# Optimization experiments

Measured on AMD Instinct MI355X. Metric: run time of the kernel, lower is better.

The kernel has to match this reference:

```python
import jax, jax.numpy as jnp
import numpy as np

B, T, XS, HS = 256, 512, 256, 256


def setup_inputs() -> dict:
    key = jax.random.key(0)
    ks = jax.random.split(key, 9)
    scale_x = np.sqrt(6.0 / (XS + HS)).astype(np.float32)  # xavier_uniform-like scale
    scale_h = np.sqrt(6.0 / (HS + HS)).astype(np.float32)
    d = {"x": jax.random.normal(ks[0], (B, T, XS), dtype=jnp.float32)}
    names = ["i", "f", "g", "o"]
    for n, kx, kh in zip(names, ks[1:5], ks[5:9]):
        d[f"wx_{n}"] = jax.random.uniform(kx, (XS, HS), jnp.float32, -scale_x, scale_x)
        d[f"wh_{n}"] = jax.random.uniform(kh, (HS, HS), jnp.float32, -scale_h, scale_h)
        d[f"bx_{n}"] = jnp.zeros((HS,), jnp.float32)
        d[f"bh_{n}"] = jnp.zeros((HS,), jnp.float32)
    return d


def reference(x, wx_i, bx_i, wh_i, bh_i, wx_f, bx_f, wh_f, bh_f,
              wx_g, bx_g, wh_g, bh_g, wx_o, bx_o, wh_o, bh_o):
    bs, ts, xs = x.shape
    hs = wx_i.shape[1]
    # Fuse the 4 input projections and 4 hidden projections into 2 GEMMs
    # (identical math to 8 separate matmuls).
    Wx = jnp.concatenate([wx_i, wx_f, wx_g, wx_o], axis=1)      # [xs, 4hs]
    Wh = jnp.concatenate([wh_i, wh_f, wh_g, wh_o], axis=1)      # [hs, 4hs]
    b = jnp.concatenate([bx_i + bh_i, bx_f + bh_f, bx_g + bh_g, bx_o + bh_o])

    # Precompute all input projections in one big GEMM: [bs, ts, 4hs]
    x_proj = jnp.einsum('btx,xg->btg', x, Wx) + b

    def step(carry, xt_proj):
        h, c = carry
        gates = xt_proj + h @ Wh                      # [bs, 4hs]
        i_t = jax.nn.sigmoid(gates[:, 0 * hs:1 * hs])
        f_t = jax.nn.sigmoid(gates[:, 1 * hs:2 * hs])
        g_t = jnp.tanh(gates[:, 2 * hs:3 * hs])
        o_t = jax.nn.sigmoid(gates[:, 3 * hs:4 * hs])
        c_new = f_t * c + i_t * g_t
        h_new = o_t * jnp.tanh(c_new)
        return (h_new, c_new), None

    h0 = jnp.zeros((bs, hs), x.dtype)
    c0 = jnp.zeros((bs, hs), x.dtype)
    (h_t, c_t), _ = jax.lax.scan(step, (h0, c0), jnp.swapaxes(x_proj, 0, 1))
    return (h_t, c_t)
```

## Files before the change

kernel.cpp:

```cpp
#include <hip/hip_runtime.h>
#include <hip/hip_bf16.h>

#define BB   256
#define TT   512
#define XSZ  256
#define HSZ  256

typedef __bf16 bf16_t;
typedef __attribute__((ext_vector_type(8))) __bf16 bf16x8;
typedef __attribute__((ext_vector_type(4))) float  f32x4;
typedef __attribute__((ext_vector_type(4))) unsigned uint4v;

__device__ __forceinline__ f32x4 splat4(float v) { f32x4 r = {v, v, v, v}; return r; }

__global__ void prep_bias(const float* bx0, const float* bh0, const float* bx1, const float* bh1,
                          const float* bx2, const float* bh2, const float* bx3, const float* bh3,
                          float* bias) {
  const float* bxs[4] = {bx0, bx1, bx2, bx3};
  const float* bhs[4] = {bh0, bh1, bh2, bh3};
  int g = blockIdx.x, c = threadIdx.x;
  bias[g * 256 + c] = bxs[g][c] + bhs[g][c];
}

__global__ void prep_wtf(const float* wx0, const float* wh0, const float* wx1, const float* wh1,
                         const float* wx2, const float* wh2, const float* wx3, const float* wh3,
                         bf16_t* Wtf) {
  const float* whs[4] = {wh0, wh1, wh2, wh3};
  const float* wxs[4] = {wx0, wx1, wx2, wx3};
  int id = blockIdx.x * 256 + threadIdx.x;
  int L  = id & 63;
  int kt = (id >> 6) & 15;
  int nt = (id >> 10) & 1;
  int w  = (id >> 11) & 7;
  int j  = (id >> 14) & 3;
  int tc   = L & 15;
  int gate = tc & 3;
  int hc   = j * 64 + w * 8 + nt * 4 + (tc >> 2);
  int k0   = kt * 32 + (L >> 4) * 8;
  const float* src = (k0 < 256) ? (whs[gate] + (size_t)k0 * 256 + hc)
                                : (wxs[gate] + (size_t)(k0 - 256) * 256 + hc);
  bf16x8 v;
#pragma unroll
  for (int i = 0; i < 8; ++i) v[i] = (__bf16)src[(size_t)i * 256];
  reinterpret_cast<bf16x8*>(Wtf)[id] = v;
}

__global__ void prep_xbf(const float* __restrict__ x, bf16_t* __restrict__ xb) {
  size_t id = (size_t)blockIdx.x * 256 + threadIdx.x;
  const float* p = x + id * 8;
  f32x4 lo = *reinterpret_cast<const f32x4*>(p);
  f32x4 hi = *reinterpret_cast<const f32x4*>(p + 4);
  bf16x8 v;
#pragma unroll
  for (int i = 0; i < 4; ++i) { v[i] = (__bf16)lo[i]; v[i + 4] = (__bf16)hi[i]; }
  reinterpret_cast<bf16x8*>(xb)[id] = v;
}

template <bool XBF>
__global__ __launch_bounds__(512, 2)
void lstm_seq(const void* __restrict__ xsrc, const bf16_t* __restrict__ Wtf,
              const float* __restrict__ bias, unsigned* __restrict__ hseq,
              float* __restrict__ out)
{
  __shared__ __align__(16) char hxl[2][8192];

  const int tid  = threadIdx.x;
  const int w    = tid >> 6;
  const int lane = tid & 63;
  const int l15  = lane & 15, l4 = lane >> 4;
  const int bid  = blockIdx.x;
  const int g    = bid >> 2, j = bid & 3;
  const int b0   = g * 16;
  const int gate = l15 & 3;
  const int hcg  = l15 >> 2;
  const bool isg = (gate == 2);

  const float*  xf32 = (const float*)xsrc;
  const bf16_t* xbf  = (const bf16_t*)xsrc;

  const char* wbase = (const char*)Wtf + (size_t)(j * 256 + w * 32) * 1024 + lane * 16;
  bf16x8 Bh[2][8], Bx[2][8];
#pragma unroll
  for (int nt = 0; nt < 2; ++nt)
#pragma unroll
    for (int kt = 0; kt < 8; ++kt) {
      Bh[nt][kt] = *reinterpret_cast<const bf16x8*>(wbase + (nt * 16 + kt) * 1024);
      Bx[nt][kt] = *reinterpret_cast<const bf16x8*>(wbase + (nt * 16 + 8 + kt) * 1024);
    }

  float bias_v[2];
#pragma unroll
  for (int nt = 0; nt < 2; ++nt)
    bias_v[nt] = bias[gate * 256 + j * 64 + w * 8 + nt * 4 + hcg];

  f32x4 cst0 = {0.f, 0.f, 0.f, 0.f};
  f32x4 cst1 = {0.f, 0.f, 0.f, 0.f};

  f32x4 acc_x0 = splat4(bias_v[0]);
  f32x4 acc_x1 = splat4(bias_v[1]);
#pragma unroll
  for (int k8 = 0; k8 < 8; ++k8) {
    bf16x8 a;
    if constexpr (XBF) {
      a = *reinterpret_cast<const bf16x8*>(
          xbf + (size_t)(b0 + l15) * (TT * XSZ) + k8 * 32 + l4 * 8);
    } else {
      const float* xp = xf32 + (size_t)(b0 + l15) * (TT * XSZ) + k8 * 32 + l4 * 8;
      f32x4 lo = *reinterpret_cast<const f32x4*>(xp);
      f32x4 hi = *reinterpret_cast<const f32x4*>(xp + 4);
#pragma unroll
      for (int i = 0; i < 4; ++i) { a[i] = (__bf16)lo[i]; a[i + 4] = (__bf16)hi[i]; }
    }
    acc_x0 = __builtin_amdgcn_mfma_f32_16x16x32_bf16(a, Bx[0][k8], acc_x0, 0, 0, 0);
    acc_x1 = __builtin_amdgcn_mfma_f32_16x16x32_bf16(a, Bx[1][k8], acc_x1, 0, 0, 0);
  }

#pragma unroll 1
  for (int t = 0; t < TT; ++t) {
    f32x4 acc0 = acc_x0;
    f32x4 acc1 = acc_x1;

    if (t > 0) {
      const unsigned* hp = hseq + (size_t)(t & 1) * 65536
                         + (size_t)(b0 + l15) * HSZ + w * 32 + l4 * 8;
      const unsigned tg = (unsigned)t;
      uint4v A, B;
      for (;;) {
        asm volatile("global_load_dwordx4 %0, %2, off sc0 sc1\n\t"
                     "global_load_dwordx4 %1, %2, off offset:16 sc0 sc1\n\t"
                     "s_waitcnt vmcnt(0)"
                     : "=&v"(A), "=&v"(B) : "v"(hp) : "memory");
        bool ok = ((A[0] >> 16) == tg) & ((A[1] >> 16) == tg) &
                  ((A[2] >> 16) == tg) & ((A[3] >> 16) == tg) &
                  ((B[0] >> 16) == tg) & ((B[1] >> 16) == tg) &
                  ((B[2] >> 16) == tg) & ((B[3] >> 16) == tg);
        if (__all((int)ok)) break;
        __builtin_amdgcn_s_sleep(1);
      }
      __builtin_amdgcn_sched_barrier(0);
      unsigned p0 = (A[0] & 0xFFFFu) | (A[1] << 16);
      unsigned p1 = (A[2] & 0xFFFFu) | (A[3] << 16);
      unsigned p2 = (B[0] & 0xFFFFu) | (B[1] << 16);
      unsigned p3 = (B[2] & 0xFFFFu) | (B[3] << 16);
      uint4v pk = {p0, p1, p2, p3};
      *reinterpret_cast<uint4v*>(hxl[t & 1] + w * 1024 + lane * 16) = pk;
    }
    __syncthreads();

    if (t > 0) {
#pragma unroll
      for (int kt = 0; kt < 8; ++kt) {
        bf16x8 a = *reinterpret_cast<const bf16x8*>(hxl[t & 1] + kt * 1024 + lane * 16);
        acc0 = __builtin_amdgcn_mfma_f32_16x16x32_bf16(a, Bh[0][kt], acc0, 0, 0, 0);
        acc1 = __builtin_amdgcn_mfma_f32_16x16x32_bf16(a, Bh[1][kt], acc1, 0, 0, 0);
      }
    }

    float hsel[2], csel[2];
#pragma unroll
    for (int nt = 0; nt < 2; ++nt) {
      f32x4 acc = nt ? acc1 : acc0;
      f32x4 av;
#pragma unroll
      for (int r = 0; r < 4; ++r) {
        float p = isg ? 2.f * acc[r] : acc[r];
        float s = 1.f / (1.f + __expf(-p));
        av[r] = isg ? (2.f * s - 1.f) : s;
      }
      f32x4 bv, v0, v1, c0, c1;
#pragma unroll
      for (int r = 0; r < 4; ++r) bv[r] = __shfl_xor(av[r], 1);
#pragma unroll
      for (int r = 0; r < 4; ++r) {
        v0[r] = (gate & 1) ? bv[r] : av[r];
        v1[r] = (gate & 1) ? av[r] : bv[r];
      }
#pragma unroll
      for (int r = 0; r < 4; ++r) { c0[r] = __shfl_xor(v0[r], 2); c1[r] = __shfl_xor(v1[r], 2); }
      f32x4 hv;
      f32x4 cs = nt ? cst1 : cst0;
#pragma unroll
      for (int r = 0; r < 4; ++r) {
        float iv = (gate & 2) ? c0[r] : v0[r];
        float fv = (gate & 2) ? c1[r] : v1[r];
        float gv = (gate & 2) ? v0[r] : c0[r];
        float ov = (gate & 2) ? v1[r] : c1[r];
        float cn = fv * cs[r] + iv * gv;
        cs[r] = cn;
        float s2 = 1.f / (1.f + __expf(-2.f * cn));
        hv[r] = ov * (2.f * s2 - 1.f);
      }
      if (nt) cst1 = cs; else cst0 = cs;
      float hs = (gate == 0) ? hv[0] : (gate == 1) ? hv[1] : (gate == 2) ? hv[2] : hv[3];
      float cc = (gate == 0) ? cs[0] : (gate == 1) ? cs[1] : (gate == 2) ? cs[2] : cs[3];
      hsel[nt] = hs;
      csel[nt] = cc;
    }

    if (t + 1 < TT) {
#pragma unroll
      for (int nt = 0; nt < 2; ++nt) {
        __bf16 hb16 = (__bf16)hsel[nt];
        unsigned hv = ((unsigned)(t + 1) << 16)
                    | (unsigned)__builtin_bit_cast(unsigned short, hb16);
        unsigned* hp2 = hseq + (size_t)((t + 1) & 1) * 65536
                      + (size_t)(b0 + l4 * 4 + gate) * HSZ
                      + (j * 64 + w * 8 + nt * 4 + hcg);
        asm volatile("global_store_dword %0, %1, off sc0 sc1" :: "v"(hp2), "v"(hv) : "memory");
      }

      acc_x0 = splat4(bias_v[0]);
      acc_x1 = splat4(bias_v[1]);
#pragma unroll
      for (int k8 = 0; k8 < 8; ++k8) {
        bf16x8 a;
        if constexpr (XBF) {
          a = *reinterpret_cast<const bf16x8*>(
              xbf + (size_t)(b0 + l15) * (TT * XSZ) + (size_t)(t + 1) * XSZ + k8 * 32 + l4 * 8);
        } else {
          const float* xp = xf32 + (size_t)(b0 + l15) * (TT * XSZ)
                          + (size_t)(t + 1) * XSZ + k8 * 32 + l4 * 8;
          f32x4 lo = *reinterpret_cast<const f32x4*>(xp);
          f32x4 hi = *reinterpret_cast<const f32x4*>(xp + 4);
#pragma unroll
          for (int i = 0; i < 4; ++i) { a[i] = (__bf16)lo[i]; a[i + 4] = (__bf16)hi[i]; }
        }
        acc_x0 = __builtin_amdgcn_mfma_f32_16x16x32_bf16(a, Bx[0][k8], acc_x0, 0, 0, 0);
        acc_x1 = __builtin_amdgcn_mfma_f32_16x16x32_bf16(a, Bx[1][k8], acc_x1, 0, 0, 0);
      }
    } else {
#pragma unroll
      for (int nt = 0; nt < 2; ++nt) {
        float* op = out + (size_t)(b0 + l4 * 4 + gate) * HSZ
                  + (j * 64 + w * 8 + nt * 4 + hcg);
        op[0] = hsel[nt];
        op[(size_t)BB * HSZ] = csel[nt];
      }
    }
  }
}

extern "C" void kernel_launch(void* const* d_in, const int* in_sizes, int n_in,
                              void* d_out, int out_size, void* d_ws, size_t ws_size,
                              hipStream_t stream) {
  const float* x = (const float*)d_in[0];
  const float *wx[4], *wh[4], *bx[4], *bh[4];
  for (int g = 0; g < 4; ++g) {
    wx[g] = (const float*)d_in[1 + 4 * g];
    wh[g] = (const float*)d_in[2 + 4 * g];
    bx[g] = (const float*)d_in[3 + 4 * g];
    bh[g] = (const float*)d_in[4 + 4 * g];
  }

  char* ws = (char*)d_ws;
  float*    bias = (float*)ws;
  bf16_t*   Wtf  = (bf16_t*)(ws + 4096);
  unsigned* hseq = (unsigned*)(ws + 4096 + 1048576);
  bf16_t*   xbf  = (bf16_t*)(ws + 4096 + 1048576 + 524288);
  const size_t need_xbf = 4096 + 1048576 + 524288 + (size_t)BB * TT * XSZ * 2;

  prep_bias<<<dim3(4), dim3(256), 0, stream>>>(bx[0], bh[0], bx[1], bh[1],
                                               bx[2], bh[2], bx[3], bh[3], bias);
  prep_wtf<<<dim3(256), dim3(256), 0, stream>>>(wx[0], wh[0], wx[1], wh[1],
                                                wx[2], wh[2], wx[3], wh[3], Wtf);
  if (ws_size >= need_xbf) {
    prep_xbf<<<dim3((BB * TT * XSZ / 8) / 256), dim3(256), 0, stream>>>(x, xbf);
    lstm_seq<true><<<dim3(64), dim3(512), 0, stream>>>(xbf, Wtf, bias, hseq,
                                                       (float*)d_out);
  } else {
    lstm_seq<false><<<dim3(64), dim3(512), 0, stream>>>(x, Wtf, bias, hseq,
                                                        (float*)d_out);
  }
}
```

Measured before the change: 2.227 ms.

## Split hidden dimension across 8 blocks per batch group and stage Wx in LDS

The hidden-column work is split across 8 blocks per 16-row batch group instead of 4, doubling the grid to 128 blocks so each wave handles one 16-column MFMA tile instead of two. The input-projection weights move from registers into a 64 KB LDS buffer, and accumulation alternates between two accumulators to break MFMA dependency chains. This shortens the per-step critical path. In exchange it doubles the number of producers taking part in the global-memory h exchange, adds LDS reads for Wx every step, and uses much more shared memory per block.

```diff
diff --git a/kernel.cpp b/kernel.cpp
--- a/kernel.cpp
+++ b/kernel.cpp
@@ -27,16 +27,15 @@
                          bf16_t* Wtf) {
   const float* whs[4] = {wh0, wh1, wh2, wh3};
   const float* wxs[4] = {wx0, wx1, wx2, wx3};
-  int id = blockIdx.x * 256 + threadIdx.x;
-  int L  = id & 63;
-  int kt = (id >> 6) & 15;
-  int nt = (id >> 10) & 1;
-  int w  = (id >> 11) & 7;
-  int j  = (id >> 14) & 3;
+  int id  = blockIdx.x * 256 + threadIdx.x;
+  int L   = id & 63;
+  int kts = (id >> 6) & 15;
+  int w   = (id >> 10) & 7;
+  int j   = (id >> 13) & 7;
   int tc   = L & 15;
   int gate = tc & 3;
-  int hc   = j * 64 + w * 8 + nt * 4 + (tc >> 2);
-  int k0   = kt * 32 + (L >> 4) * 8;
+  int hc   = j * 32 + w * 4 + (tc >> 2);
+  int k0   = kts * 32 + (L >> 4) * 8;
   const float* src = (k0 < 256) ? (whs[gate] + (size_t)k0 * 256 + hc)
                                 : (wxs[gate] + (size_t)(k0 - 256) * 256 + hc);
   bf16x8 v;
@@ -62,6 +61,7 @@
               const float* __restrict__ bias, unsigned* __restrict__ hseq,
               float* __restrict__ out)
 {
+  __shared__ __align__(16) char bxlds[65536];
   __shared__ __align__(16) char hxl[2][8192];
 
   const int tid  = threadIdx.x;
@@ -69,7 +69,7 @@
   const int lane = tid & 63;
   const int l15  = lane & 15, l4 = lane >> 4;
   const int bid  = blockIdx.x;
-  const int g    = bid >> 2, j = bid & 3;
+  const int g    = bid >> 3, j = bid & 7;
   const int b0   = g * 16;
   const int gate = l15 & 3;
   const int hcg  = l15 >> 2;
@@ -78,26 +78,25 @@
   const float*  xf32 = (const float*)xsrc;
   const bf16_t* xbf  = (const bf16_t*)xsrc;
 
-  const char* wbase = (const char*)Wtf + (size_t)(j * 256 + w * 32) * 1024 + lane * 16;
-  bf16x8 Bh[2][8], Bx[2][8];
-#pragma unroll
-  for (int nt = 0; nt < 2; ++nt)
-#pragma unroll
-    for (int kt = 0; kt < 8; ++kt) {
-      Bh[nt][kt] = *reinterpret_cast<const bf16x8*>(wbase + (nt * 16 + kt) * 1024);
-      Bx[nt][kt] = *reinterpret_cast<const bf16x8*>(wbase + (nt * 16 + 8 + kt) * 1024);
-    }
-
-  float bias_v[2];
-#pragma unroll
-  for (int nt = 0; nt < 2; ++nt)
-    bias_v[nt] = bias[gate * 256 + j * 64 + w * 8 + nt * 4 + hcg];
-
-  f32x4 cst0 = {0.f, 0.f, 0.f, 0.f};
-  f32x4 cst1 = {0.f, 0.f, 0.f, 0.f};
-
-  f32x4 acc_x0 = splat4(bias_v[0]);
-  f32x4 acc_x1 = splat4(bias_v[1]);
+  const char* wbase = (const char*)Wtf + ((size_t)(j * 8 + w) * 16) * 1024 + lane * 16;
+  bf16x8 Bh[8];
+#pragma unroll
+  for (int kt = 0; kt < 8; ++kt)
+    Bh[kt] = *reinterpret_cast<const bf16x8*>(wbase + kt * 1024);
+#pragma unroll
+  for (int q = 0; q < 8; ++q) {
+    bf16x8 v = *reinterpret_cast<const bf16x8*>(wbase + (8 + q) * 1024);
+    *reinterpret_cast<bf16x8*>(bxlds + (w * 8 + q) * 1024 + lane * 16) = v;
+  }
+
+  const float bias_v = bias[gate * 256 + j * 32 + w * 4 + hcg];
+
+  f32x4 cst = {0.f, 0.f, 0.f, 0.f};
+
+  __syncthreads();
+
+  f32x4 axa = splat4(bias_v);
+  f32x4 axb = {0.f, 0.f, 0.f, 0.f};
 #pragma unroll
   for (int k8 = 0; k8 < 8; ++k8) {
     bf16x8 a;
@@ -111,14 +110,15 @@
 #pragma unroll
       for (int i = 0; i < 4; ++i) { a[i] = (__bf16)lo[i]; a[i + 4] = (__bf16)hi[i]; }
     }
-    acc_x0 = __builtin_amdgcn_mfma_f32_16x16x32_bf16(a, Bx[0][k8], acc_x0, 0, 0, 0);
-    acc_x1 = __builtin_amdgcn_mfma_f32_16x16x32_bf16(a, Bx[1][k8], acc_x1, 0, 0, 0);
+    bf16x8 bx = *reinterpret_cast<const bf16x8*>(bxlds + (w * 8 + k8) * 1024 + lane * 16);
+    if (k8 & 1) axb = __builtin_amdgcn_mfma_f32_16x16x32_bf16(a, bx, axb, 0, 0, 0);
+    else        axa = __builtin_amdgcn_mfma_f32_16x16x32_bf16(a, bx, axa, 0, 0, 0);
   }
 
 #pragma unroll 1
   for (int t = 0; t < TT; ++t) {
-    f32x4 acc0 = acc_x0;
-    f32x4 acc1 = acc_x1;
+    f32x4 acc_a = axa;
+    f32x4 acc_b = axb;
 
     if (t > 0) {
       const unsigned* hp = hseq + (size_t)(t & 1) * 65536
@@ -151,66 +151,54 @@
 #pragma unroll
       for (int kt = 0; kt < 8; ++kt) {
         bf16x8 a = *reinterpret_cast<const bf16x8*>(hxl[t & 1] + kt * 1024 + lane * 16);
-        acc0 = __builtin_amdgcn_mfma_f32_16x16x32_bf16(a, Bh[0][kt], acc0, 0, 0, 0);
-        acc1 = __builtin_amdgcn_mfma_f32_16x16x32_bf16(a, Bh[1][kt], acc1, 0, 0, 0);
+        if (kt & 1) acc_b = __builtin_amdgcn_mfma_f32_16x16x32_bf16(a, Bh[kt], acc_b, 0, 0, 0);
+        else        acc_a = __builtin_amdgcn_mfma_f32_16x16x32_bf16(a, Bh[kt], acc_a, 0, 0, 0);
       }
     }
 
-    float hsel[2], csel[2];
-#pragma unroll
-    for (int nt = 0; nt < 2; ++nt) {
-      f32x4 acc = nt ? acc1 : acc0;
-      f32x4 av;
-#pragma unroll
-      for (int r = 0; r < 4; ++r) {
-        float p = isg ? 2.f * acc[r] : acc[r];
-        float s = 1.f / (1.f + __expf(-p));
-        av[r] = isg ? (2.f * s - 1.f) : s;
-      }
-      f32x4 bv, v0, v1, c0, c1;
-#pragma unroll
-      for (int r = 0; r < 4; ++r) bv[r] = __shfl_xor(av[r], 1);
-#pragma unroll
-      for (int r = 0; r < 4; ++r) {
-        v0[r] = (gate & 1) ? bv[r] : av[r];
-        v1[r] = (gate & 1) ? av[r] : bv[r];
-      }
-#pragma unroll
-      for (int r = 0; r < 4; ++r) { c0[r] = __shfl_xor(v0[r], 2); c1[r] = __shfl_xor(v1[r], 2); }
-      f32x4 hv;
-      f32x4 cs = nt ? cst1 : cst0;
-#pragma unroll
-      for (int r = 0; r < 4; ++r) {
-        float iv = (gate & 2) ? c0[r] : v0[r];
-        float fv = (gate & 2) ? c1[r] : v1[r];
-        float gv = (gate & 2) ? v0[r] : c0[r];
-        float ov = (gate & 2) ? v1[r] : c1[r];
-        float cn = fv * cs[r] + iv * gv;
-        cs[r] = cn;
-        float s2 = 1.f / (1.f + __expf(-2.f * cn));
-        hv[r] = ov * (2.f * s2 - 1.f);
-      }
-      if (nt) cst1 = cs; else cst0 = cs;
-      float hs = (gate == 0) ? hv[0] : (gate == 1) ? hv[1] : (gate == 2) ? hv[2] : hv[3];
-      float cc = (gate == 0) ? cs[0] : (gate == 1) ? cs[1] : (gate == 2) ? cs[2] : cs[3];
-      hsel[nt] = hs;
-      csel[nt] = cc;
-    }
+    f32x4 av;
+#pragma unroll
+    for (int r = 0; r < 4; ++r) {
+      float vr = acc_a[r] + acc_b[r];
+      float p  = isg ? 2.f * vr : vr;
+      float s  = 1.f / (1.f + __expf(-p));
+      av[r] = isg ? (2.f * s - 1.f) : s;
+    }
+    f32x4 bv, v0, v1, c0, c1;
+#pragma unroll
+    for (int r = 0; r < 4; ++r) bv[r] = __shfl_xor(av[r], 1);
+#pragma unroll
+    for (int r = 0; r < 4; ++r) {
+      v0[r] = (gate & 1) ? bv[r] : av[r];
+      v1[r] = (gate & 1) ? av[r] : bv[r];
+    }
+#pragma unroll
+    for (int r = 0; r < 4; ++r) { c0[r] = __shfl_xor(v0[r], 2); c1[r] = __shfl_xor(v1[r], 2); }
+    f32x4 hv;
+#pragma unroll
+    for (int r = 0; r < 4; ++r) {
+      float iv = (gate & 2) ? c0[r] : v0[r];
+      float fv = (gate & 2) ? c1[r] : v1[r];
+      float gv = (gate & 2) ? v0[r] : c0[r];
+      float ov = (gate & 2) ? v1[r] : c1[r];
+      float cn = fv * cst[r] + iv * gv;
+      cst[r] = cn;
+      float s2 = 1.f / (1.f + __expf(-2.f * cn));
+      hv[r] = ov * (2.f * s2 - 1.f);
+    }
+    float hsel = (gate == 0) ? hv[0] : (gate == 1) ? hv[1] : (gate == 2) ? hv[2] : hv[3];
+    float csel = (gate == 0) ? cst[0] : (gate == 1) ? cst[1] : (gate == 2) ? cst[2] : cst[3];
 
     if (t + 1 < TT) {
-#pragma unroll
-      for (int nt = 0; nt < 2; ++nt) {
-        __bf16 hb16 = (__bf16)hsel[nt];
-        unsigned hv = ((unsigned)(t + 1) << 16)
-                    | (unsigned)__builtin_bit_cast(unsigned short, hb16);
-        unsigned* hp2 = hseq + (size_t)((t + 1) & 1) * 65536
-                      + (size_t)(b0 + l4 * 4 + gate) * HSZ
-                      + (j * 64 + w * 8 + nt * 4 + hcg);
-        asm volatile("global_store_dword %0, %1, off sc0 sc1" :: "v"(hp2), "v"(hv) : "memory");
-      }
-
-      acc_x0 = splat4(bias_v[0]);
-      acc_x1 = splat4(bias_v[1]);
+      __bf16 hb16 = (__bf16)hsel;
+      unsigned hvd = ((unsigned)(t + 1) << 16)
+                   | (unsigned)__builtin_bit_cast(unsigned short, hb16);
+      unsigned* hp2 = hseq + (size_t)((t + 1) & 1) * 65536
+                    + (size_t)(b0 + l4 * 4 + gate) * HSZ + (j * 32 + w * 4 + hcg);
+      asm volatile("global_store_dword %0, %1, off sc0 sc1" :: "v"(hp2), "v"(hvd) : "memory");
+
+      axa = splat4(bias_v);
+      axb = f32x4{0.f, 0.f, 0.f, 0.f};
 #pragma unroll
       for (int k8 = 0; k8 < 8; ++k8) {
         bf16x8 a;
@@ -225,17 +213,14 @@
 #pragma unroll
           for (int i = 0; i < 4; ++i) { a[i] = (__bf16)lo[i]; a[i + 4] = (__bf16)hi[i]; }
         }
-        acc_x0 = __builtin_amdgcn_mfma_f32_16x16x32_bf16(a, Bx[0][k8], acc_x0, 0, 0, 0);
-        acc_x1 = __builtin_amdgcn_mfma_f32_16x16x32_bf16(a, Bx[1][k8], acc_x1, 0, 0, 0);
+        bf16x8 bx = *reinterpret_cast<const bf16x8*>(bxlds + (w * 8 + k8) * 1024 + lane * 16);
+        if (k8 & 1) axb = __builtin_amdgcn_mfma_f32_16x16x32_bf16(a, bx, axb, 0, 0, 0);
+        else        axa = __builtin_amdgcn_mfma_f32_16x16x32_bf16(a, bx, axa, 0, 0, 0);
       }
     } else {
-#pragma unroll
-      for (int nt = 0; nt < 2; ++nt) {
-        float* op = out + (size_t)(b0 + l4 * 4 + gate) * HSZ
-                  + (j * 64 + w * 8 + nt * 4 + hcg);
-        op[0] = hsel[nt];
-        op[(size_t)BB * HSZ] = csel[nt];
-      }
+      float* op = out + (size_t)(b0 + l4 * 4 + gate) * HSZ + (j * 32 + w * 4 + hcg);
+      op[0] = hsel;
+      op[(size_t)BB * HSZ] = csel;
     }
   }
 }
@@ -265,10 +250,10 @@
                                                 wx[2], wh[2], wx[3], wh[3], Wtf);
   if (ws_size >= need_xbf) {
     prep_xbf<<<dim3((BB * TT * XSZ / 8) / 256), dim3(256), 0, stream>>>(x, xbf);
-    lstm_seq<true><<<dim3(64), dim3(512), 0, stream>>>(xbf, Wtf, bias, hseq,
-                                                       (float*)d_out);
+    lstm_seq<true><<<dim3(128), dim3(512), 0, stream>>>(xbf, Wtf, bias, hseq,
+                                                        (float*)d_out);
   } else {
-    lstm_seq<false><<<dim3(64), dim3(512), 0, stream>>>(x, Wtf, bias, hseq,
-                                                        (float*)d_out);
-  }
-}
+    lstm_seq<false><<<dim3(128), dim3(512), 0, stream>>>(x, Wtf, bias, hseq,
+                                                         (float*)d_out);
+  }
+}
```

New measurement: 1.877 ms. 15.7% less time.
